# Kernel optimization log

Hardware: AMD Instinct MI355X
Metric: run time of the kernel (lower is better)

The kernel has to match this reference:

```python
import jax, jax.numpy as jnp
import numpy as np

HEADS = 4
OUT_DIM = 64
NEG_SLOPE = 0.2


def setup_inputs() -> dict:
    key = jax.random.key(0)
    k1, k2, k3, k4 = jax.random.split(key, 4)
    n, in_dim = 4096, 256
    x = jax.random.normal(k1, (n, in_dim), dtype=jnp.float32)
    adj = jax.random.randint(k2, (n, n), 0, 2, dtype=jnp.int32)
    # lin: in_dim -> heads*out_dim (no bias), stored as [in_dim, heads*out_dim]
    W = jax.random.normal(k3, (in_dim, HEADS * OUT_DIM), dtype=jnp.float32) * 0.05
    # att_weight: [heads, 2*out_dim]
    att = jax.random.normal(k4, (HEADS, 2 * OUT_DIM), dtype=jnp.float32) * 0.05
    return {"x": x, "adj": adj, "W": W, "att": att}


def reference(x, adj, W, att):
    n = x.shape[0]
    h = (x @ W).reshape(n, HEADS, OUT_DIM)  # [n, H, D]
    # scores[i,j,h] = att[h] . cat(h_i, h_j) = <h_i, a_src[h]> + <h_j, a_dst[h]>
    a_src, a_dst = att[:, :OUT_DIM], att[:, OUT_DIM:]
    e_src = jnp.einsum('nhd,hd->nh', h, a_src)  # [n, H]
    e_dst = jnp.einsum('nhd,hd->nh', h, a_dst)  # [n, H]
    scores = e_src[:, None, :] + e_dst[None, :, :]  # [n, n, H]
    scores = jax.nn.leaky_relu(scores, negative_slope=NEG_SLOPE)
    mask = (adj > 0)[:, :, None]  # [n, n, 1]
    scores = jnp.where(mask, scores, -jnp.inf)
    alpha = jax.nn.softmax(scores, axis=1)  # softmax over neighbors j
    # h_prime[i,h,d] = sum_j alpha[i,j,h] * h[j,h,d]
    h_prime = jnp.einsum('ijh,jhd->ihd', alpha, h)
    return h_prime.reshape(n, HEADS * OUT_DIM)
```

## Files before the change

kernel.cpp:

```cpp
#include <hip/hip_runtime.h>
#include <hip/hip_bf16.h>

#define HEADS 4
#define ODIM 64
#define HD 256
#define NEG_SLOPE 0.2f

typedef __attribute__((ext_vector_type(8))) short bf16x8;
typedef __attribute__((ext_vector_type(4))) float floatx4;
typedef __attribute__((ext_vector_type(2))) float floatx2;

__global__ __launch_bounds__(256) void pack_xw(const float* __restrict__ x,
                                               const float* __restrict__ W,
                                               __hip_bfloat16* __restrict__ xh,
                                               __hip_bfloat16* __restrict__ xl,
                                               __hip_bfloat16* __restrict__ wh,
                                               __hip_bfloat16* __restrict__ wl,
                                               int K, int nxb) {
    const int b = blockIdx.x;
    const int Kc = K >> 5;
    if (b < nxb) {
        const int g = b * 256 + threadIdx.x;
        const int lane = g & 63, frag = g >> 6;
        const int kc = frag % Kc, mc = frag / Kc;
        const int l16 = lane & 15, q = lane >> 4;
        const float* src = x + (size_t)(mc * 16 + l16) * K + kc * 32 + q * 8;
        const float4 v0 = *(const float4*)src;
        const float4 v1 = *(const float4*)(src + 4);
        const float vv[8] = {v0.x, v0.y, v0.z, v0.w, v1.x, v1.y, v1.z, v1.w};
        union { __hip_bfloat16 b[8]; bf16x8 v; } H, L;
        #pragma unroll
        for (int p = 0; p < 8; ++p) {
            H.b[p] = __float2bfloat16(vv[p]);
            L.b[p] = __float2bfloat16(vv[p] - __bfloat162float(H.b[p]));
        }
        *(bf16x8*)&xh[(size_t)frag * 512 + lane * 8] = H.v;
        *(bf16x8*)&xl[(size_t)frag * 512 + lane * 8] = L.v;
    } else {
        const int g = (b - nxb) * 256 + threadIdx.x;
        const int lane = g & 63, frag = g >> 6;
        const int kc = frag % Kc, nc = frag / Kc;
        const int l16 = lane & 15, q = lane >> 4;
        union { __hip_bfloat16 b[8]; bf16x8 v; } H, L;
        #pragma unroll
        for (int p = 0; p < 8; ++p) {
            const float w = W[(size_t)(kc * 32 + q * 8 + p) * HD + nc * 16 + l16];
            H.b[p] = __float2bfloat16(w);
            L.b[p] = __float2bfloat16(w - __bfloat162float(H.b[p]));
        }
        *(bf16x8*)&wh[(size_t)frag * 512 + lane * 8] = H.v;
        *(bf16x8*)&wl[(size_t)frag * 512 + lane * 8] = L.v;
    }
}

__global__ __launch_bounds__(128) void gemm_fused(
    const __hip_bfloat16* __restrict__ xh, const __hip_bfloat16* __restrict__ xl,
    const __hip_bfloat16* __restrict__ wh, const __hip_bfloat16* __restrict__ wl,
    const float* __restrict__ att, float2* __restrict__ esrc, float2* __restrict__ edst,
    __hip_bfloat16* __restrict__ hbB, int n, int K) {

    __shared__ __hip_bfloat16 T[64][40];

    const int tid = threadIdx.x, wave = tid >> 6, lane = tid & 63;
    const int q = lane >> 4, l16 = lane & 15;
    const int m0 = blockIdx.x * 32;
    const int head = blockIdx.y;
    const int Kc = K >> 5;
    const int mc = (m0 >> 4) + wave;

    floatx4 acc[4] = {{0.f,0.f,0.f,0.f},{0.f,0.f,0.f,0.f},{0.f,0.f,0.f,0.f},{0.f,0.f,0.f,0.f}};

    const __hip_bfloat16* Axh = xh + (size_t)mc * Kc * 512 + lane * 8;
    const __hip_bfloat16* Axl = xl + (size_t)mc * Kc * 512 + lane * 8;
    const __hip_bfloat16* Bwh = wh + lane * 8;
    const __hip_bfloat16* Bwl = wl + lane * 8;
    #pragma unroll 2
    for (int kc = 0; kc < Kc; ++kc) {
        const bf16x8 ah = *(const bf16x8*)(Axh + (size_t)kc * 512);
        const bf16x8 al = *(const bf16x8*)(Axl + (size_t)kc * 512);
        bf16x8 bh[4], bl[4];
        #pragma unroll
        for (int nt = 0; nt < 4; ++nt) {
            const size_t fo = (size_t)((head * 4 + nt) * Kc + kc) * 512;
            bh[nt] = *(const bf16x8*)(Bwh + fo);
            bl[nt] = *(const bf16x8*)(Bwl + fo);
        }
        #pragma unroll
        for (int nt = 0; nt < 4; ++nt)
            acc[nt] = __builtin_amdgcn_mfma_f32_16x16x32_bf16(ah, bh[nt], acc[nt], 0, 0, 0);
        #pragma unroll
        for (int nt = 0; nt < 4; ++nt)
            acc[nt] = __builtin_amdgcn_mfma_f32_16x16x32_bf16(ah, bl[nt], acc[nt], 0, 0, 0);
        #pragma unroll
        for (int nt = 0; nt < 4; ++nt)
            acc[nt] = __builtin_amdgcn_mfma_f32_16x16x32_bf16(al, bh[nt], acc[nt], 0, 0, 0);
    }

    float as_v[4], ad_v[4];
    #pragma unroll
    for (int nt = 0; nt < 4; ++nt) {
        as_v[nt] = att[head * 2 * ODIM + nt * 16 + l16];
        ad_v[nt] = att[head * 2 * ODIM + ODIM + nt * 16 + l16];
    }
    #pragma unroll
    for (int r = 0; r < 4; ++r) {
        float ps = 0.f, pd = 0.f;
        #pragma unroll
        for (int nt = 0; nt < 4; ++nt) {
            ps = fmaf(acc[nt][r], as_v[nt], ps);
            pd = fmaf(acc[nt][r], ad_v[nt], pd);
        }
        #pragma unroll
        for (int m = 1; m <= 8; m <<= 1) {
            ps += __shfl_xor(ps, m, 64);
            pd += __shfl_xor(pd, m, 64);
        }
        if (l16 == 0) {
            const int i = m0 + wave * 16 + q * 4 + r;
            esrc[head * n + i] = make_float2(__expf(ps), __expf(NEG_SLOPE * ps));
            edst[head * n + i] = make_float2(__expf(pd), __expf(NEG_SLOPE * pd));
        }
    }

    #pragma unroll
    for (int nt = 0; nt < 4; ++nt) {
        union { __hip_bfloat16 b[4]; uint2 u; } pk;
        #pragma unroll
        for (int r = 0; r < 4; ++r) pk.b[r] = __float2bfloat16(acc[nt][r]);
        *(uint2*)&T[nt * 16 + l16][wave * 16 + q * 4] = pk.u;
    }
    __syncthreads();

    #pragma unroll
    for (int ffi = 0; ffi < 2; ++ffi) {
        const int f = wave + ffi * 2;
        const bf16x8 v = *(const bf16x8*)&T[f * 16 + l16][q * 8];
        const size_t frag = ((size_t)head * (n >> 5) + (m0 >> 5)) * 4 + f;
        *(bf16x8*)&hbB[frag * 512 + lane * 8] = v;
    }
}

__global__ __launch_bounds__(256, 4) void aggregate(
    const int* __restrict__ adj, const float2* __restrict__ esrc,
    const float2* __restrict__ edst, const __hip_bfloat16* __restrict__ hbB,
    float* __restrict__ outsp, float* __restrict__ densp, int n, int KR) {

    const int tid = threadIdx.x;
    const int wave = tid >> 6, lane = tid & 63;
    const int q = lane >> 4, l16 = lane & 15;
    const int i0 = blockIdx.x * 32;
    const int K0 = blockIdx.y * KR;

    floatx2 es12[2];
    #pragma unroll
    for (int mt = 0; mt < 2; ++mt) {
        const float2 e = esrc[wave * n + i0 + mt * 16 + l16];
        es12[mt][0] = e.x; es12[mt][1] = e.y;
    }

    union { short s[8]; bf16x8 v; } bones;
    #pragma unroll
    for (int p = 0; p < 8; ++p) bones.s[p] = (l16 == 0) ? (short)0x3F80 : (short)0;

    floatx4 acc[2][4];
    floatx4 accd[2];
    #pragma unroll
    for (int mt = 0; mt < 2; ++mt) {
        accd[mt] = (floatx4){0.f, 0.f, 0.f, 0.f};
        #pragma unroll
        for (int nt = 0; nt < 4; ++nt) acc[mt][nt] = (floatx4){0.f, 0.f, 0.f, 0.f};
    }

    const int* arow0 = adj + (size_t)(i0 + l16) * n + K0 + q * 8;
    const int* arow1 = arow0 + (size_t)16 * n;
    const float2* edp = edst + (size_t)wave * n + K0 + q * 8;
    const __hip_bfloat16* hb = hbB + ((size_t)wave * (n >> 5) + (K0 >> 5)) * 4 * 512 + lane * 8;

    const int NSTEP = KR >> 5;

    int4 aj[4];
    {
        const int4* p0 = (const int4*)arow0;
        const int4* p1 = (const int4*)arow1;
        aj[0] = p0[0]; aj[1] = p0[1]; aj[2] = p1[0]; aj[3] = p1[1];
    }

    for (int s = 0; s < NSTEP; ++s) {
        float4 ced[4]; bf16x8 cbf[4];
        {
            const float4* ep = (const float4*)(edp + (size_t)s * 32);
            ced[0] = ep[0]; ced[1] = ep[1]; ced[2] = ep[2]; ced[3] = ep[3];
            #pragma unroll
            for (int nt = 0; nt < 4; ++nt)
                cbf[nt] = *(const bf16x8*)&hb[((size_t)s * 4 + nt) * 512];
        }

        const int* av = (const int*)aj;
        #pragma unroll
        for (int mt = 0; mt < 2; ++mt) {
            union { unsigned int u[4]; bf16x8 v; } af;
            #pragma unroll
            for (int p = 0; p < 4; ++p) {
                const float4 e = ced[p];
                floatx2 e0; e0[0] = e.x; e0[1] = e.y;
                floatx2 e1; e1[0] = e.z; e1[1] = e.w;
                const floatx2 pa = es12[mt] * e0;
                const floatx2 pb = es12[mt] * e1;
                float wa = fmaxf(pa[0], pa[1]);
                float wb = fmaxf(pb[0], pb[1]);
                wa = (av[mt * 8 + 2 * p]     > 0) ? wa : 0.0f;
                wb = (av[mt * 8 + 2 * p + 1] > 0) ? wb : 0.0f;
                af.u[p] = __builtin_amdgcn_perm(__float_as_uint(wb), __float_as_uint(wa),
                                                0x07060302u);
            }
            #pragma unroll
            for (int nt = 0; nt < 4; ++nt)
                acc[mt][nt] = __builtin_amdgcn_mfma_f32_16x16x32_bf16(af.v, cbf[nt], acc[mt][nt], 0, 0, 0);
            accd[mt] = __builtin_amdgcn_mfma_f32_16x16x32_bf16(af.v, bones.v, accd[mt], 0, 0, 0);
        }

        const int sn = (s + 1 < NSTEP) ? s + 1 : s;
        {
            const int4* p0 = (const int4*)(arow0 + (size_t)sn * 32);
            const int4* p1 = (const int4*)(arow1 + (size_t)sn * 32);
            aj[0] = p0[0]; aj[1] = p0[1]; aj[2] = p1[0]; aj[3] = p1[1];
        }
    }

    const size_t sOut = (size_t)blockIdx.y * n * HD;
    #pragma unroll
    for (int mt = 0; mt < 2; ++mt)
        #pragma unroll
        for (int nt = 0; nt < 4; ++nt)
            #pragma unroll
            for (int r = 0; r < 4; ++r)
                outsp[sOut + (size_t)(i0 + mt * 16 + q * 4 + r) * HD + wave * ODIM + nt * 16 + l16] = acc[mt][nt][r];
    if (l16 == 0) {
        #pragma unroll
        for (int mt = 0; mt < 2; ++mt)
            #pragma unroll
            for (int r = 0; r < 4; ++r)
                densp[((size_t)blockIdx.y * n + i0 + mt * 16 + q * 4 + r) * HEADS + wave] = accd[mt][r];
    }
}

__global__ __launch_bounds__(256) void normalize(const float* __restrict__ outsp,
                                                 const float* __restrict__ densp,
                                                 float* __restrict__ out, int n, int splits) {
    const int g = blockIdx.x * 256 + threadIdx.x;
    const int i = g >> 6;
    const int c4 = (g & 63) * 4;
    const int head = c4 >> 6;
    float den = 0.f;
    for (int s = 0; s < splits; ++s) den += densp[((size_t)s * n + i) * HEADS + head];
    float4 v = {0.f, 0.f, 0.f, 0.f};
    for (int s = 0; s < splits; ++s) {
        const float4 t = *(const float4*)&outsp[(size_t)s * n * HD + (size_t)i * HD + c4];
        v.x += t.x; v.y += t.y; v.z += t.z; v.w += t.w;
    }
    const float inv = 1.0f / den;
    v.x *= inv; v.y *= inv; v.z *= inv; v.w *= inv;
    *(float4*)&out[(size_t)i * HD + c4] = v;
}

extern "C" void kernel_launch(void* const* d_in, const int* in_sizes, int n_in,
                              void* d_out, int out_size, void* d_ws, size_t ws_size,
                              hipStream_t stream) {
    const float* x   = (const float*)d_in[0];
    const int*   adj = (const int*)d_in[1];
    const float* W   = (const float*)d_in[2];
    const float* att = (const float*)d_in[3];
    float* out = (float*)d_out;

    const int in_dim = in_sizes[2] / HD;
    const int n = in_sizes[0] / in_dim;

    char* ws = (char*)d_ws;
    size_t off = 0;
    auto alloc = [&](size_t bytes) -> void* {
        void* p = ws + off; off += (bytes + 255) & ~(size_t)255; return p;
    };
    __hip_bfloat16* xh = (__hip_bfloat16*)alloc((size_t)n * in_dim * 2);
    __hip_bfloat16* xl = (__hip_bfloat16*)alloc((size_t)n * in_dim * 2);
    __hip_bfloat16* wh = (__hip_bfloat16*)alloc((size_t)in_dim * HD * 2);
    __hip_bfloat16* wl = (__hip_bfloat16*)alloc((size_t)in_dim * HD * 2);
    float2* esrc = (float2*)alloc((size_t)HEADS * n * 8);
    float2* edst = (float2*)alloc((size_t)HEADS * n * 8);
    __hip_bfloat16* hbB = (__hip_bfloat16*)alloc((size_t)n * HD * 2);

    const size_t outB = (size_t)n * HD * 4, denB = (size_t)n * HEADS * 4;
    int splits = (ws_size >= off + 8 * (outB + denB)) ? 8 : 4;
    float* densp = (float*)alloc((size_t)splits * denB);
    float* outsp = (float*)alloc((size_t)splits * outB);

    const int nxb = (n / 16) * (in_dim / 32) * 64 / 256;
    const int nwb = (HD / 16) * (in_dim / 32) * 64 / 256;
    pack_xw<<<nxb + nwb, 256, 0, stream>>>(x, W, xh, xl, wh, wl, in_dim, nxb);
    gemm_fused<<<dim3(n / 32, HEADS), 128, 0, stream>>>(xh, xl, wh, wl, att, esrc, edst, hbB, n, in_dim);
    aggregate<<<dim3(n / 32, splits), 256, 0, stream>>>(adj, esrc, edst, hbB, outsp, densp, n, n / splits);
    normalize<<<n * 64 / 256, 256, 0, stream>>>(outsp, densp, out, n, splits);
}
```

Measured before the change: 168.2 us.

## Stage adjacency bitmask and edst in LDS, double-buffer hbB fragments in aggregate

The aggregate kernel now loads its whole 32x512 adjacency tile up front, packs it into an LDS bitmask, and stages the edst slice in LDS. The main loop then reads the mask and edst from LDS and masks the packed bf16 weights with bit operations. The hbB fragment loads are double-buffered across steps. Splits is fixed at 8 and launch bounds drop to 3 blocks per CU. The aim is to replace scattered per-step global int32 adjacency reads with one coalesced burst and to hide hbB latency. In exchange it uses more LDS and registers, and removes the fallback check on workspace size.

```diff
diff --git a/kernel.cpp b/kernel.cpp
--- a/kernel.cpp
+++ b/kernel.cpp
@@ -5,6 +5,7 @@
 #define ODIM 64
 #define HD 256
 #define NEG_SLOPE 0.2f
+#define SPLITS 8
 
 typedef __attribute__((ext_vector_type(8))) short bf16x8;
 typedef __attribute__((ext_vector_type(4))) float floatx4;
@@ -140,10 +141,13 @@
     }
 }
 
-__global__ __launch_bounds__(256, 4) void aggregate(
+__global__ __launch_bounds__(256, 3) void aggregate(
     const int* __restrict__ adj, const float2* __restrict__ esrc,
     const float2* __restrict__ edst, const __hip_bfloat16* __restrict__ hbB,
     float* __restrict__ outsp, float* __restrict__ densp, int n, int KR) {
+
+    __shared__ unsigned char bitsL[32][68];
+    __shared__ float2 edL[HEADS][512];
 
     const int tid = threadIdx.x;
     const int wave = tid >> 6, lane = tid & 63;
@@ -151,6 +155,28 @@
     const int i0 = blockIdx.x * 32;
     const int K0 = blockIdx.y * KR;
 
+    {
+        const int r0 = i0 + wave * 8;
+        #pragma unroll
+        for (int rr = 0; rr < 8; ++rr) {
+            const int4* ap = (const int4*)(adj + (size_t)(r0 + rr) * n + K0 + lane * 8);
+            const int4 a = ap[0], b = ap[1];
+            unsigned int by = (unsigned int)(a.x > 0)
+                            | ((unsigned int)(a.y > 0) << 1)
+                            | ((unsigned int)(a.z > 0) << 2)
+                            | ((unsigned int)(a.w > 0) << 3)
+                            | ((unsigned int)(b.x > 0) << 4)
+                            | ((unsigned int)(b.y > 0) << 5)
+                            | ((unsigned int)(b.z > 0) << 6)
+                            | ((unsigned int)(b.w > 0) << 7);
+            bitsL[wave * 8 + rr][lane] = (unsigned char)by;
+        }
+    }
+    for (int t = tid; t < HEADS * 512; t += 256) {
+        const int h = t >> 9, j = t & 511;
+        edL[h][j] = edst[(size_t)h * n + K0 + j];
+    }
+
     floatx2 es12[2];
     #pragma unroll
     for (int mt = 0; mt < 2; ++mt) {
@@ -171,60 +197,57 @@
         for (int nt = 0; nt < 4; ++nt) acc[mt][nt] = (floatx4){0.f, 0.f, 0.f, 0.f};
     }
 
-    const int* arow0 = adj + (size_t)(i0 + l16) * n + K0 + q * 8;
-    const int* arow1 = arow0 + (size_t)16 * n;
-    const float2* edp = edst + (size_t)wave * n + K0 + q * 8;
+    __syncthreads();
+
     const __hip_bfloat16* hb = hbB + ((size_t)wave * (n >> 5) + (K0 >> 5)) * 4 * 512 + lane * 8;
-
     const int NSTEP = KR >> 5;
 
-    int4 aj[4];
-    {
-        const int4* p0 = (const int4*)arow0;
-        const int4* p1 = (const int4*)arow1;
-        aj[0] = p0[0]; aj[1] = p0[1]; aj[2] = p1[0]; aj[3] = p1[1];
-    }
-
-    for (int s = 0; s < NSTEP; ++s) {
-        float4 ced[4]; bf16x8 cbf[4];
-        {
-            const float4* ep = (const float4*)(edp + (size_t)s * 32);
-            ced[0] = ep[0]; ced[1] = ep[1]; ced[2] = ep[2]; ced[3] = ep[3];
-            #pragma unroll
-            for (int nt = 0; nt < 4; ++nt)
-                cbf[nt] = *(const bf16x8*)&hb[((size_t)s * 4 + nt) * 512];
-        }
-
-        const int* av = (const int*)aj;
+    auto loadBF = [&](int s, bf16x8* dst) {
+        #pragma unroll
+        for (int nt = 0; nt < 4; ++nt)
+            dst[nt] = *(const bf16x8*)&hb[((size_t)s * 4 + nt) * 512];
+    };
+
+    auto computeStep = [&](int s, const bf16x8* bfr) {
+        const unsigned int bm0 = (*(const unsigned int*)&bitsL[l16][s * 4] >> (q * 8)) & 0xFFu;
+        const unsigned int bm1 = (*(const unsigned int*)&bitsL[16 + l16][s * 4] >> (q * 8)) & 0xFFu;
+        const float4* ep = (const float4*)&edL[wave][s * 32 + q * 8];
+        const float4 e01 = ep[0], e23 = ep[1], e45 = ep[2], e67 = ep[3];
+        floatx2 ed[8];
+        ed[0][0]=e01.x; ed[0][1]=e01.y;  ed[1][0]=e01.z; ed[1][1]=e01.w;
+        ed[2][0]=e23.x; ed[2][1]=e23.y;  ed[3][0]=e23.z; ed[3][1]=e23.w;
+        ed[4][0]=e45.x; ed[4][1]=e45.y;  ed[5][0]=e45.z; ed[5][1]=e45.w;
+        ed[6][0]=e67.x; ed[6][1]=e67.y;  ed[7][0]=e67.z; ed[7][1]=e67.w;
         #pragma unroll
         for (int mt = 0; mt < 2; ++mt) {
+            const unsigned int bm = mt ? bm1 : bm0;
             union { unsigned int u[4]; bf16x8 v; } af;
             #pragma unroll
             for (int p = 0; p < 4; ++p) {
-                const float4 e = ced[p];
-                floatx2 e0; e0[0] = e.x; e0[1] = e.y;
-                floatx2 e1; e1[0] = e.z; e1[1] = e.w;
-                const floatx2 pa = es12[mt] * e0;
-                const floatx2 pb = es12[mt] * e1;
-                float wa = fmaxf(pa[0], pa[1]);
-                float wb = fmaxf(pb[0], pb[1]);
-                wa = (av[mt * 8 + 2 * p]     > 0) ? wa : 0.0f;
-                wb = (av[mt * 8 + 2 * p + 1] > 0) ? wb : 0.0f;
+                const floatx2 pa = es12[mt] * ed[2 * p];
+                const floatx2 pb = es12[mt] * ed[2 * p + 1];
+                const float wa = fmaxf(pa[0], pa[1]);
+                const float wb = fmaxf(pb[0], pb[1]);
+                const unsigned int mm = ((bm >> (2 * p)) & 1u) * 0xFFFFu
+                                      | ((bm >> (2 * p + 1)) & 1u) * 0xFFFF0000u;
                 af.u[p] = __builtin_amdgcn_perm(__float_as_uint(wb), __float_as_uint(wa),
-                                                0x07060302u);
+                                                0x07060302u) & mm;
             }
             #pragma unroll
             for (int nt = 0; nt < 4; ++nt)
-                acc[mt][nt] = __builtin_amdgcn_mfma_f32_16x16x32_bf16(af.v, cbf[nt], acc[mt][nt], 0, 0, 0);
+                acc[mt][nt] = __builtin_amdgcn_mfma_f32_16x16x32_bf16(af.v, bfr[nt], acc[mt][nt], 0, 0, 0);
             accd[mt] = __builtin_amdgcn_mfma_f32_16x16x32_bf16(af.v, bones.v, accd[mt], 0, 0, 0);
         }
-
-        const int sn = (s + 1 < NSTEP) ? s + 1 : s;
-        {
-            const int4* p0 = (const int4*)(arow0 + (size_t)sn * 32);
-            const int4* p1 = (const int4*)(arow1 + (size_t)sn * 32);
-            aj[0] = p0[0]; aj[1] = p0[1]; aj[2] = p1[0]; aj[3] = p1[1];
-        }
+    };
+
+    bf16x8 bA[4], bB[4];
+    loadBF(0, bA);
+    loadBF(1, bB);
+    for (int s = 0; s < NSTEP; s += 2) {
+        computeStep(s, bA);
+        if (s + 2 < NSTEP) loadBF(s + 2, bA);
+        computeStep(s + 1, bB);
+        if (s + 3 < NSTEP) loadBF(s + 3, bB);
     }
 
     const size_t sOut = (size_t)blockIdx.y * n * HD;
@@ -289,14 +312,13 @@
     __hip_bfloat16* hbB = (__hip_bfloat16*)alloc((size_t)n * HD * 2);
 
     const size_t outB = (size_t)n * HD * 4, denB = (size_t)n * HEADS * 4;
-    int splits = (ws_size >= off + 8 * (outB + denB)) ? 8 : 4;
-    float* densp = (float*)alloc((size_t)splits * denB);
-    float* outsp = (float*)alloc((size_t)splits * outB);
+    float* densp = (float*)alloc((size_t)SPLITS * denB);
+    float* outsp = (float*)alloc((size_t)SPLITS * outB);
 
     const int nxb = (n / 16) * (in_dim / 32) * 64 / 256;
     const int nwb = (HD / 16) * (in_dim / 32) * 64 / 256;
     pack_xw<<<nxb + nwb, 256, 0, stream>>>(x, W, xh, xl, wh, wl, in_dim, nxb);
     gemm_fused<<<dim3(n / 32, HEADS), 128, 0, stream>>>(xh, xl, wh, wl, att, esrc, edst, hbB, n, in_dim);
-    aggregate<<<dim3(n / 32, splits), 256, 0, stream>>>(adj, esrc, edst, hbB, outsp, densp, n, n / splits);
-    normalize<<<n * 64 / 256, 256, 0, stream>>>(outsp, densp, out, n, splits);
-}
+    aggregate<<<dim3(n / 32, SPLITS), 256, 0, stream>>>(adj, esrc, edst, hbB, outsp, densp, n, n / SPLITS);
+    normalize<<<n * 64 / 256, 256, 0, stream>>>(outsp, densp, out, n, SPLITS);
+}
```

Result: faster. 144.0 us (-14.4%).
